# Kernel tuning notes

Measured on AMD Instinct MI355X. Metric: run time of the kernel, lower is better.

The kernel has to match this reference:

```python
import jax, jax.numpy as jnp
import numpy as np
from jax import lax

B, T, D, H = 32, 512, 1024, 1024


def setup_inputs() -> dict:
    key = jax.random.key(0)
    ks = jax.random.split(key, 6)
    inp = jax.random.normal(ks[0], (B, T, D), jnp.float32)
    attention_mask = jnp.ones((B, T), jnp.float32)
    nonzero_index = jax.random.randint(ks[1], (B, 1), 0, T)
    # Stacked gate weights, gate order (i, f, g, o); equivalent to 8 separate Linears.
    W_x = jax.random.normal(ks[2], (D, 4 * H), jnp.float32) * 0.02
    W_h = jax.random.normal(ks[3], (H, 4 * H), jnp.float32) * 0.02
    b_x = jax.random.normal(ks[4], (4 * H,), jnp.float32) * 0.02
    b_h = jax.random.normal(ks[5], (4 * H,), jnp.float32) * 0.02
    return {"input": inp, "attention_mask": attention_mask, "nonzero_index": nonzero_index,
            "W_x": W_x, "W_h": W_h, "b_x": b_x, "b_h": b_h}


def reference(input, attention_mask, nonzero_index, W_x, W_h, b_x, b_h):
    # Precompute all input-side gate projections in one big matmul: [B,T,4H]
    x_gates = jnp.einsum('btd,dg->btg', input, W_x) + b_x + b_h

    def step(carry, xg):
        h, c = carry                       # [B,H] each
        g = xg + h @ W_h                   # [B,4H]
        i, f, gg, o = jnp.split(g, 4, axis=-1)
        i = jax.nn.sigmoid(i)
        f = jax.nn.sigmoid(f)
        gg = jnp.tanh(gg)
        o = jax.nn.sigmoid(o)
        c = f * c + i * gg
        h = o * jnp.tanh(c)
        return (h, c), (h, c)

    h0 = jnp.zeros((B, H), x_gates.dtype)
    c0 = jnp.zeros((B, H), x_gates.dtype)
    _, (hs, cs) = lax.scan(step, (h0, c0), jnp.swapaxes(x_gates, 0, 1))  # [T,B,H]
    hts = jnp.swapaxes(hs, 0, 1)  # [B,T,H]
    cts = jnp.swapaxes(cs, 0, 1)
    # cls token gathered BEFORE masking (matches original order)
    cls_token = jnp.take_along_axis(hts, nonzero_index[:, :, None], axis=1)[:, 0, :]
    hts = hts * attention_mask[:, :, None]
    cts = cts * attention_mask[:, :, None]
    return (hts, hts, cts, cls_token)
```

## Files before the change

kernel.cpp:

```cpp
#include <hip/hip_runtime.h>
#include <stdint.h>


typedef _Float16 f16;
typedef __attribute__((ext_vector_type(8))) _Float16 f16x8;
typedef __attribute__((ext_vector_type(4))) float f32x4;
typedef __attribute__((ext_vector_type(4))) unsigned int u32x4;

#define NG 2
#define NW 8
#define HBYTES (2 * NG * 2048 * 16)

__device__ __forceinline__ float sigm(float v){ return 1.f/(1.f+__expf(-v)); }
__device__ __forceinline__ float tanh_(float v){ return 2.f/(1.f+__expf(-2.f*v)) - 1.f; }

__device__ __forceinline__ u32x4 ld16_sc(const void* p) {
  u32x4 r;
  asm volatile("global_load_dwordx4 %0, %1, off sc0 sc1" : "=v"(r) : "v"(p));
  return r;
}
__device__ __forceinline__ void st2_sc(void* p, uint32_t v) {
  asm volatile("global_store_short %0, %1, off sc0 sc1" :: "v"(p), "v"(v) : "memory");
}

__global__ __launch_bounds__(512, 1) void lstm_kernel(
    const float* __restrict__ xin, const float* __restrict__ amask,
    const int* __restrict__ nzidx, const float* __restrict__ Wx,
    const float* __restrict__ Wh, const float* __restrict__ bx,
    const float* __restrict__ bh, float* __restrict__ out,
    uint32_t* __restrict__ ws)
{
  __shared__ __align__(16) f16 Wl[128][64][8];
  __shared__ __align__(16) float pl[2][NW][2][64][4];

  const int tid  = threadIdx.x;
  const int lane = tid & 63;
  const int wid  = tid >> 6;
  const int r    = blockIdx.x & 127;
  const int G    = blockIdx.x >> 7;
  const int hbase = r * 8;

  uint8_t* hb8 = (uint8_t*)ws;

  for (int f = wid; f < 128; f += NW) {
    const int side = f >> 6, kf = (f >> 1) & 31, nt = f & 1;
    const int c16 = lane & 15, kslot_ = lane >> 4;
    const int g = nt * 2 + (c16 >> 3);
    const int gcol = g * 1024 + hbase + (c16 & 7);
    const int k0 = kf * 32 + kslot_ * 8;
    const float* Wsrc = side ? Wh : Wx;
    f16x8 v;
#pragma unroll
    for (int e = 0; e < 8; ++e) v[e] = (f16)Wsrc[(size_t)(k0 + e) * 4096 + gcol];
    *(f16x8*)&Wl[f][lane][0] = v;
  }
  const int b  = tid >> 3;
  const int hc = tid & 7;
  const int b_glob = G * 16 + b;
  float bias[4] = {0.f, 0.f, 0.f, 0.f};
  float cval = 0.f, mv_cur = 0.f;
  int myidx = -1;
  if (tid < 128) {
#pragma unroll
    for (int g = 0; g < 4; ++g) {
      const int gcol = g * 1024 + hbase + hc;
      bias[g] = bx[gcol] + bh[gcol];
    }
    myidx = nzidx[b_glob];
    mv_cur = amask[(size_t)b_glob * 512];
  }
  const int bb = lane & 15, kslot = lane >> 4;
  f32x4 xf[4][2];
  {
    const size_t xrow = ((size_t)(G * 16 + bb) * 512) * 1024;
#pragma unroll
    for (int q = 0; q < 4; ++q) {
      const float* xs = xin + xrow + (wid * 4 + q) * 32 + kslot * 8;
      xf[q][0] = *(const f32x4*)xs;
      xf[q][1] = *(const f32x4*)(xs + 4);
    }
  }
  __syncthreads();

  bool gave_up = false;
#pragma unroll 1
  for (int t = 0; t < 512; ++t) {
    const int ppl = t & 1;
    f16x8 xa[4];
#pragma unroll
    for (int q = 0; q < 4; ++q) {
      f16x8 a;
#pragma unroll
      for (int i = 0; i < 4; ++i) { a[i] = (f16)xf[q][0][i]; a[i + 4] = (f16)xf[q][1][i]; }
      xa[q] = a;
    }
    const uint8_t* hsrc = hb8 + ((size_t)((t & 1) * NG + G) << 15);
    uint32_t pat = 0;
    size_t aoff[4];
    u32x4 hq[4];
    if (t > 0) {
      const uint32_t tb = ((uint32_t)(t >> 1) + 1u) & 3u;
      pat = (tb & 1u) | (((tb >> 1) & 1u) << 16);
#pragma unroll
      for (int q = 0; q < 4; ++q) {
        const int rsrc = (wid * 4 + q) * 4 + kslot;
        aoff[q] = (size_t)(rsrc * 16 + bb) << 4;
        hq[q] = ld16_sc(hsrc + aoff[q]);
      }
    }
    f32x4 acc0 = {0.f,0.f,0.f,0.f}, acc1 = {0.f,0.f,0.f,0.f};
#pragma unroll
    for (int q = 0; q < 4; ++q) {
      const int kf = wid * 4 + q;
      f16x8 b0 = *(const f16x8*)&Wl[kf * 2 + 0][lane][0];
      f16x8 b1 = *(const f16x8*)&Wl[kf * 2 + 1][lane][0];
      acc0 = __builtin_amdgcn_mfma_f32_16x16x32_f16(xa[q], b0, acc0, 0, 0, 0);
      acc1 = __builtin_amdgcn_mfma_f32_16x16x32_f16(xa[q], b1, acc1, 0, 0, 0);
    }
    if (t > 0) {
      if (!gave_up) {
        bool got = false;
        int spins = 0;
        for (;;) {
          asm volatile("s_waitcnt vmcnt(0)" ::: "memory");
          __builtin_amdgcn_sched_barrier(0);
          bool ok = true;
#pragma unroll
          for (int q = 0; q < 4; ++q)
#pragma unroll
            for (int j = 0; j < 4; ++j) ok &= ((hq[q][j] & 0x00010001u) == pat);
          if (__all((int)ok)) { got = true; break; }
          if (++spins > (1 << 14)) break;
#pragma unroll
          for (int q = 0; q < 4; ++q) hq[q] = ld16_sc(hsrc + aoff[q]);
        }
        if (!got) gave_up = true;
      } else {
        asm volatile("s_waitcnt vmcnt(0)" ::: "memory");
        __builtin_amdgcn_sched_barrier(0);
      }
      if (t + 1 < 512) {
        const size_t xrow = ((size_t)(G * 16 + bb) * 512 + (size_t)(t + 1)) * 1024;
#pragma unroll
        for (int q = 0; q < 4; ++q) {
          const float* xs = xin + xrow + (wid * 4 + q) * 32 + kslot * 8;
          xf[q][0] = *(const f32x4*)xs;
          xf[q][1] = *(const f32x4*)(xs + 4);
        }
      }
#pragma unroll
      for (int q = 0; q < 4; ++q) {
        union { u32x4 u; f16x8 v; } cu; cu.u = hq[q];
        const int kf = wid * 4 + q;
        f16x8 b0 = *(const f16x8*)&Wl[64 + kf * 2 + 0][lane][0];
        f16x8 b1 = *(const f16x8*)&Wl[64 + kf * 2 + 1][lane][0];
        acc0 = __builtin_amdgcn_mfma_f32_16x16x32_f16(cu.v, b0, acc0, 0, 0, 0);
        acc1 = __builtin_amdgcn_mfma_f32_16x16x32_f16(cu.v, b1, acc1, 0, 0, 0);
      }
    } else {
      const size_t xrow = ((size_t)(G * 16 + bb) * 512 + 1) * 1024;
#pragma unroll
      for (int q = 0; q < 4; ++q) {
        const float* xs = xin + xrow + (wid * 4 + q) * 32 + kslot * 8;
        xf[q][0] = *(const f32x4*)xs;
        xf[q][1] = *(const f32x4*)(xs + 4);
      }
    }
    *(f32x4*)&pl[ppl][wid][0][lane][0] = acc0;
    *(f32x4*)&pl[ppl][wid][1][lane][0] = acc1;
    __syncthreads();
    if (tid < 128) {
      float s[4];
#pragma unroll
      for (int g = 0; g < 4; ++g) {
        const int lp = ((g & 1) * 8 + hc) + 16 * (b >> 2);
        const int reg = b & 3;
        float v = bias[g];
#pragma unroll
        for (int w = 0; w < NW; ++w) v += pl[ppl][w][g >> 1][lp][reg];
        s[g] = v;
      }
      const float ig = sigm(s[0]);
      const float fg = sigm(s[1]);
      const float gg = tanh_(s[2]);
      const float og = sigm(s[3]);
      cval = fg * cval + ig * gg;
      const float hval = og * tanh_(cval);
      if (t < 511) {
        union { f16 f; uint16_t u; } pk; pk.f = (f16)hval;
        const uint32_t tbp = ((uint32_t)((t + 1) >> 1) + 1u) & 3u;
        const uint32_t bitv = (hc & 1) ? ((tbp >> 1) & 1u) : (tbp & 1u);
        const uint32_t val = ((uint32_t)pk.u & 0xFFFEu) | bitv;
        uint8_t* dst = hb8 + ((size_t)(((t + 1) & 1) * NG + G) << 15)
                     + ((size_t)(r * 16 + b) << 4) + (hc << 1);
        st2_sc(dst, val);
      }
      const float mval = mv_cur;
      if (t + 1 < 512) mv_cur = amask[(size_t)b_glob * 512 + (size_t)(t + 1)];
      const size_t o0 = ((size_t)b_glob * 512 + (size_t)t) * 1024 + (size_t)(hbase + hc);
      out[o0] = hval * mval;
      out[o0 + 16777216u] = hval * mval;
      out[o0 + 33554432u] = cval * mval;
      if (t == myidx) out[50331648u + (size_t)b_glob * 1024 + (size_t)(hbase + hc)] = hval;
    }
  }
}

extern "C" void kernel_launch(void* const* d_in, const int* in_sizes, int n_in,
                              void* d_out, int out_size, void* d_ws, size_t ws_size,
                              hipStream_t stream) {
  const float* xin   = (const float*)d_in[0];
  const float* amask = (const float*)d_in[1];
  const int*   nzidx = (const int*)d_in[2];
  const float* Wx    = (const float*)d_in[3];
  const float* Wh    = (const float*)d_in[4];
  const float* bx    = (const float*)d_in[5];
  const float* bh    = (const float*)d_in[6];
  float* out = (float*)d_out;
  uint32_t* ws = (uint32_t*)d_ws;

  hipMemsetAsync(d_ws, 0, HBYTES, stream);

  void* args[] = {(void*)&xin, (void*)&amask, (void*)&nzidx, (void*)&Wx,
                  (void*)&Wh, (void*)&bx, (void*)&bh, (void*)&out, (void*)&ws};
  hipError_t e = hipLaunchCooperativeKernel((const void*)lstm_kernel, dim3(256), dim3(512),
                                            args, 0, stream);
  if (e != hipSuccess) {
    lstm_kernel<<<dim3(256), dim3(512), 0, stream>>>(xin, amask, nzidx, Wx, Wh, bx, bh, out, ws);
  }
}
```

Measured before the change: 2.098 ms.

## Batch output stores over four steps and reorder loads around spin wait

The per-step masked h/c output stores are buffered in registers for four timesteps and written in a batch during the spin-wait phase of a later step, with a final flush after the loop. The next-step x prefetch moves ahead of the input-side MFMAs, and the h polling loads move after a sched barrier, with waves 2 and up briefly sleeping to stagger polling traffic. The aim is to take global output stores off the serial critical path and cut contention on the inter-block h exchange. In exchange it uses more registers, and the sleeps could add latency.

```diff
diff --git a/kernel.cpp b/kernel.cpp
--- a/kernel.cpp
+++ b/kernel.cpp
@@ -69,6 +69,7 @@
     myidx = nzidx[b_glob];
     mv_cur = amask[(size_t)b_glob * 512];
   }
+  float hmb0=0.f,hmb1=0.f,hmb2=0.f,hmb3=0.f, cmb0=0.f,cmb1=0.f,cmb2=0.f,cmb3=0.f;
   const int bb = lane & 15, kslot = lane >> 4;
   f32x4 xf[4][2];
   {
@@ -94,18 +95,13 @@
       for (int i = 0; i < 4; ++i) { a[i] = (f16)xf[q][0][i]; a[i + 4] = (f16)xf[q][1][i]; }
       xa[q] = a;
     }
-    const uint8_t* hsrc = hb8 + ((size_t)((t & 1) * NG + G) << 15);
-    uint32_t pat = 0;
-    size_t aoff[4];
-    u32x4 hq[4];
-    if (t > 0) {
-      const uint32_t tb = ((uint32_t)(t >> 1) + 1u) & 3u;
-      pat = (tb & 1u) | (((tb >> 1) & 1u) << 16);
+    if (t + 1 < 512) {
+      const size_t xrow = ((size_t)(G * 16 + bb) * 512 + (size_t)(t + 1)) * 1024;
 #pragma unroll
       for (int q = 0; q < 4; ++q) {
-        const int rsrc = (wid * 4 + q) * 4 + kslot;
-        aoff[q] = (size_t)(rsrc * 16 + bb) << 4;
-        hq[q] = ld16_sc(hsrc + aoff[q]);
+        const float* xs = xin + xrow + (wid * 4 + q) * 32 + kslot * 8;
+        xf[q][0] = *(const f32x4*)xs;
+        xf[q][1] = *(const f32x4*)(xs + 4);
       }
     }
     f32x4 acc0 = {0.f,0.f,0.f,0.f}, acc1 = {0.f,0.f,0.f,0.f};
@@ -117,7 +113,20 @@
       acc0 = __builtin_amdgcn_mfma_f32_16x16x32_f16(xa[q], b0, acc0, 0, 0, 0);
       acc1 = __builtin_amdgcn_mfma_f32_16x16x32_f16(xa[q], b1, acc1, 0, 0, 0);
     }
+    __builtin_amdgcn_sched_barrier(0);
     if (t > 0) {
+      const uint8_t* hsrc = hb8 + ((size_t)((t & 1) * NG + G) << 15);
+      const uint32_t tb = ((uint32_t)(t >> 1) + 1u) & 3u;
+      const uint32_t pat = (tb & 1u) | (((tb >> 1) & 1u) << 16);
+      size_t aoff[4];
+      u32x4 hq[4];
+      if (wid >= 2) __builtin_amdgcn_s_sleep(2);
+#pragma unroll
+      for (int q = 0; q < 4; ++q) {
+        const int rsrc = (wid * 4 + q) * 4 + kslot;
+        aoff[q] = (size_t)(rsrc * 16 + bb) << 4;
+        hq[q] = ld16_sc(hsrc + aoff[q]);
+      }
       if (!gave_up) {
         bool got = false;
         int spins = 0;
@@ -139,14 +148,17 @@
         asm volatile("s_waitcnt vmcnt(0)" ::: "memory");
         __builtin_amdgcn_sched_barrier(0);
       }
-      if (t + 1 < 512) {
-        const size_t xrow = ((size_t)(G * 16 + bb) * 512 + (size_t)(t + 1)) * 1024;
-#pragma unroll
-        for (int q = 0; q < 4; ++q) {
-          const float* xs = xin + xrow + (wid * 4 + q) * 32 + kslot * 8;
-          xf[q][0] = *(const f32x4*)xs;
-          xf[q][1] = *(const f32x4*)(xs + 4);
-        }
+      if (tid < 128 && (t & 3) == 0) {
+        const size_t ob0 = ((size_t)b_glob * 512 + (size_t)(t - 4)) * 1024
+                         + (size_t)(hbase + hc);
+        out[ob0]                    = hmb0; out[ob0 + 16777216u]        = hmb0;
+        out[ob0 + 33554432u]        = cmb0;
+        out[ob0 + 1024]             = hmb1; out[ob0 + 1024 + 16777216u] = hmb1;
+        out[ob0 + 1024 + 33554432u] = cmb1;
+        out[ob0 + 2048]             = hmb2; out[ob0 + 2048 + 16777216u] = hmb2;
+        out[ob0 + 2048 + 33554432u] = cmb2;
+        out[ob0 + 3072]             = hmb3; out[ob0 + 3072 + 16777216u] = hmb3;
+        out[ob0 + 3072 + 33554432u] = cmb3;
       }
 #pragma unroll
       for (int q = 0; q < 4; ++q) {
@@ -156,14 +168,6 @@
         f16x8 b1 = *(const f16x8*)&Wl[64 + kf * 2 + 1][lane][0];
         acc0 = __builtin_amdgcn_mfma_f32_16x16x32_f16(cu.v, b0, acc0, 0, 0, 0);
         acc1 = __builtin_amdgcn_mfma_f32_16x16x32_f16(cu.v, b1, acc1, 0, 0, 0);
-      }
-    } else {
-      const size_t xrow = ((size_t)(G * 16 + bb) * 512 + 1) * 1024;
-#pragma unroll
-      for (int q = 0; q < 4; ++q) {
-        const float* xs = xin + xrow + (wid * 4 + q) * 32 + kslot * 8;
-        xf[q][0] = *(const f32x4*)xs;
-        xf[q][1] = *(const f32x4*)(xs + 4);
       }
     }
     *(f32x4*)&pl[ppl][wid][0][lane][0] = acc0;
@@ -195,14 +199,27 @@
                      + ((size_t)(r * 16 + b) << 4) + (hc << 1);
         st2_sc(dst, val);
       }
-      const float mval = mv_cur;
+      const float hm = hval * mv_cur, cm = cval * mv_cur;
+      const int sl = t & 3;
+      if (sl == 0)      { hmb0 = hm; cmb0 = cm; }
+      else if (sl == 1) { hmb1 = hm; cmb1 = cm; }
+      else if (sl == 2) { hmb2 = hm; cmb2 = cm; }
+      else              { hmb3 = hm; cmb3 = cm; }
+      if (t == myidx)
+        out[50331648u + (size_t)b_glob * 1024 + (size_t)(hbase + hc)] = hval;
       if (t + 1 < 512) mv_cur = amask[(size_t)b_glob * 512 + (size_t)(t + 1)];
-      const size_t o0 = ((size_t)b_glob * 512 + (size_t)t) * 1024 + (size_t)(hbase + hc);
-      out[o0] = hval * mval;
-      out[o0 + 16777216u] = hval * mval;
-      out[o0 + 33554432u] = cval * mval;
-      if (t == myidx) out[50331648u + (size_t)b_glob * 1024 + (size_t)(hbase + hc)] = hval;
-    }
+    }
+  }
+  if (tid < 128) {
+    const size_t ob0 = ((size_t)b_glob * 512 + 508) * 1024 + (size_t)(hbase + hc);
+    out[ob0]                    = hmb0; out[ob0 + 16777216u]        = hmb0;
+    out[ob0 + 33554432u]        = cmb0;
+    out[ob0 + 1024]             = hmb1; out[ob0 + 1024 + 16777216u] = hmb1;
+    out[ob0 + 1024 + 33554432u] = cmb1;
+    out[ob0 + 2048]             = hmb2; out[ob0 + 2048 + 16777216u] = hmb2;
+    out[ob0 + 2048 + 33554432u] = cmb2;
+    out[ob0 + 3072]             = hmb3; out[ob0 + 3072 + 16777216u] = hmb3;
+    out[ob0 + 3072 + 33554432u] = cmb3;
   }
 }
 
```

Result: no change. 2.114 ms (+0.8%).
